# Kernel optimization log

Measured on AMD Instinct MI355X. Metric: run time of the kernel, lower is better.

Reference implementation:

```python
import jax, jax.numpy as jnp
import numpy as np

N, F_IN, H, D = 4096, 256, 8, 16  # nodes, in_features, heads, per-head dim
HD = H * D                        # 128 = out_features
NEG_SLOPE = 0.3


def _masked_softmax(w, g):
    """Replicates torch.sparse.softmax on (w*g).to_sparse() along dim=2.

    Softmax is taken over entries where g != 0 (the sparse nonzeros),
    with value w*g there; fully-masked rows densify back to all zeros.
    w, g: [H, N, N] -> attn [H, N, N].
    """
    mask = g != 0.0
    val = jnp.where(mask, w * g, jnp.float32(-1e30))
    val = val - jnp.max(val, axis=2, keepdims=True)
    e = jnp.exp(val) * mask.astype(w.dtype)
    denom = jnp.maximum(jnp.sum(e, axis=2, keepdims=True), jnp.float32(1e-30))
    return e / denom


def setup_inputs() -> dict:
    key = jax.random.key(0)
    ks = jax.random.split(key, 12)
    s = 0.05
    inputs = jax.random.normal(ks[0], (N, F_IN), dtype=jnp.float32)
    Dgraph = jax.random.randint(ks[1], (N, N), 0, 2).astype(jnp.float32)
    Sgraph = jax.random.randint(ks[2], (N, N), 0, 2).astype(jnp.float32)
    # params (torch Linear stored here as [in, out] so y = x @ W + b)
    W_w = jax.random.normal(ks[3], (F_IN, HD), dtype=jnp.float32) * s
    W_b = jax.random.normal(ks[4], (HD,), dtype=jnp.float32) * s
    wu = jax.random.normal(ks[5], (H, D, 1), dtype=jnp.float32) * s
    wv = jax.random.normal(ks[6], (H, D, 1), dtype=jnp.float32) * s
    Wcat_w = jax.random.normal(ks[7], (2 * HD, HD), dtype=jnp.float32) * s
    Wcat_b = jax.random.normal(ks[8], (HD,), dtype=jnp.float32) * s
    bias = jax.random.normal(ks[9], (1, HD), dtype=jnp.float32) * s
    proj_w = jax.random.normal(ks[10], (F_IN, HD), dtype=jnp.float32) * s
    proj_b = jax.random.normal(ks[11], (HD,), dtype=jnp.float32) * s
    return {"inputs": inputs, "Dgraph": Dgraph, "Sgraph": Sgraph,
            "W_w": W_w, "W_b": W_b, "wu": wu, "wv": wv,
            "Wcat_w": Wcat_w, "Wcat_b": Wcat_b, "bias": bias,
            "proj_w": proj_w, "proj_b": proj_b}


def reference(inputs, Dgraph, Sgraph, W_w, W_b, wu, wv, Wcat_w, Wcat_b, bias, proj_w, proj_b):
    n = inputs.shape[0]
    score = (inputs @ W_w + W_b).reshape(n, H, D).transpose(1, 0, 2)  # [H,N,D]
    f1 = jnp.einsum('hnd,hd->hn', score, wu[:, :, 0])[:, None, :]     # [H,1,N]
    f2 = jnp.einsum('hnd,hd->hn', score, wv[:, :, 0])[:, :, None]     # [H,N,1]
    logits = f1 + f2                                                  # [H,N,N]
    w = jnp.where(logits >= 0, logits, NEG_SLOPE * logits)            # leaky_relu

    D_attn = _masked_softmax(w, Dgraph[None])                         # [H,N,N]
    D_sup = jnp.einsum('hnm,hmd->hnd', D_attn, score)
    D_sup = D_sup.transpose(1, 0, 2).reshape(n, HD)

    S_attn = _masked_softmax(w, Sgraph[None])
    S_sup = jnp.einsum('hnm,hmd->hnd', S_attn, score)
    S_sup = S_sup.transpose(1, 0, 2).reshape(n, HD)

    out = jnp.concatenate([S_sup, D_sup], axis=1) @ Wcat_w + Wcat_b
    out = out + bias
    out = out + inputs @ proj_w + proj_b
    return out
```

## Files before the change

kernel.cpp:

```cpp
#include <hip/hip_runtime.h>
#include <hip/hip_bf16.h>


#define NN 4096
#define LOG2E 1.44269504088896340736f
#define NS 4
#define CHUNK 1024
#define MROW 2064

typedef short bf16x8 __attribute__((ext_vector_type(8)));
typedef float f32x4  __attribute__((ext_vector_type(4)));
typedef _Float16 h16x8 __attribute__((ext_vector_type(8)));
typedef _Float16 h16x2 __attribute__((ext_vector_type(2)));
typedef __fp16  fp16x2 __attribute__((ext_vector_type(2)));

union hu8 { unsigned int u[4]; h16x8 v; };
union hu2 { unsigned int u; h16x2 h; };

__device__ __forceinline__ unsigned short f2bf_rn(float f) {
  union { float f; unsigned int i; } v; v.f = f;
  unsigned int r = v.i + 0x7FFFu + ((v.i >> 16) & 1u);
  return (unsigned short)(r >> 16);
}
__device__ __forceinline__ unsigned int pk2(float lo, float hi) {
  fp16x2 h = __builtin_amdgcn_cvt_pkrtz(lo, hi);
  union { fp16x2 h; unsigned int u; } v; v.h = h; return v.u;
}
__device__ __forceinline__ float dot2acc(unsigned int pair, float acc) {
  hu2 p; p.u = pair;
#if __has_builtin(__builtin_amdgcn_fdot2)
  const h16x2 one2 = {(_Float16)1.f, (_Float16)1.f};
  return __builtin_amdgcn_fdot2(p.h, one2, acc, false);
#else
  return acc + (float)p.h.x + (float)p.h.y;
#endif
}
__device__ __forceinline__ unsigned int bytesel(float4 a) {
  return (a.x != 0.f ? 0x000000FFu : 0u) | (a.y != 0.f ? 0x0000FF00u : 0u)
       | (a.z != 0.f ? 0x00FF0000u : 0u) | (a.w != 0.f ? 0xFF000000u : 0u);
}

__global__ __launch_bounds__(256) void k_prep(
    const float* __restrict__ X, const float* __restrict__ Ww,
    const float* __restrict__ Wcat, const float* __restrict__ proj,
    const float* __restrict__ Wcb, const float* __restrict__ bias,
    const float* __restrict__ prb,
    unsigned short* __restrict__ Xb, unsigned short* __restrict__ WwT,
    unsigned short* __restrict__ WpT, float* __restrict__ bsum)
{
  const int tid = blockIdx.x * 256 + threadIdx.x;
  {
    const float4 a = *(const float4*)(X + (size_t)tid * 8);
    const float4 b = *(const float4*)(X + (size_t)tid * 8 + 4);
    uint4 o;
    o.x = (unsigned)f2bf_rn(a.x) | ((unsigned)f2bf_rn(a.y) << 16);
    o.y = (unsigned)f2bf_rn(a.z) | ((unsigned)f2bf_rn(a.w) << 16);
    o.z = (unsigned)f2bf_rn(b.x) | ((unsigned)f2bf_rn(b.y) << 16);
    o.w = (unsigned)f2bf_rn(b.z) | ((unsigned)f2bf_rn(b.w) << 16);
    *(uint4*)(Xb + (size_t)tid * 8) = o;
  }
  if (tid < 32768) {
    int c = tid & 127, k = tid >> 7;
    WwT[c * 256 + k] = f2bf_rn(Ww[k * 128 + c]);
  }
  if (tid < 65536) {
    int c = tid & 127, k = tid >> 7;
    float v = (k < 256) ? Wcat[k * 128 + c] : proj[(k - 256) * 128 + c];
    WpT[c * 512 + k] = f2bf_rn(v);
  }
  if (tid < 128) bsum[tid] = Wcb[tid] + bias[tid] + prb[tid];
}

__global__ __launch_bounds__(256) void k_cvt(
    const float* __restrict__ Dg, const float* __restrict__ Sg,
    unsigned char* __restrict__ mDS)
{
  const size_t tid = (size_t)blockIdx.x * 256 + threadIdx.x;
  const size_t off = tid * 8;
  const float4 da = *(const float4*)(Dg + off);
  const float4 db = *(const float4*)(Dg + off + 4);
  const float4 sa = *(const float4*)(Sg + off);
  const float4 sb = *(const float4*)(Sg + off + 4);
  uint4 o;
  o.x = bytesel(da); o.y = bytesel(db);
  o.z = bytesel(sa); o.w = bytesel(sb);
  *(uint4*)(mDS + tid * 16) = o;
}

__global__ __launch_bounds__(512) void k_score(
    const unsigned short* __restrict__ Xb, const unsigned short* __restrict__ WwT,
    const float* __restrict__ Wb, const float* __restrict__ wu,
    const float* __restrict__ wv,
    unsigned short* __restrict__ scT, float* __restrict__ f2,
    unsigned short* __restrict__ E1p, unsigned short* __restrict__ E3p)
{
  const int n0 = blockIdx.x * 16;
  const int h = threadIdx.x >> 6, lane = threadIdx.x & 63;
  const int mr = lane & 15, grp = lane >> 4;
  const unsigned short* ap  = Xb  + (size_t)(n0 + mr) * 256;
  const unsigned short* bpp = WwT + (size_t)(h * 16 + mr) * 256;
  f32x4 acc = {0.f, 0.f, 0.f, 0.f};
  #pragma unroll
  for (int ks = 0; ks < 8; ++ks) {
    bf16x8 a = *(const bf16x8*)(ap  + ks * 32 + grp * 8);
    bf16x8 b = *(const bf16x8*)(bpp + ks * 32 + grp * 8);
    acc = __builtin_amdgcn_mfma_f32_16x16x32_bf16(a, b, acc, 0, 0, 0);
  }
  const float wb = Wb[h * 16 + mr];
  float sc[4];
  #pragma unroll
  for (int r = 0; r < 4; ++r) sc[r] = acc[r] + wb;

  {
    uint2 st;
    st.x = pk2(sc[0], sc[1]);
    st.y = pk2(sc[2], sc[3]);
    *(uint2*)(scT + (size_t)(h * 16 + mr) * NN + n0 + grp * 4) = st;
  }

  const float uw = wu[h * 16 + mr], vw = wv[h * 16 + mr];
  float t1[4], t2[4];
  #pragma unroll
  for (int r = 0; r < 4; ++r) { t1[r] = sc[r] * uw; t2[r] = sc[r] * vw; }
  #pragma unroll
  for (int m = 1; m < 16; m <<= 1) {
    #pragma unroll
    for (int r = 0; r < 4; ++r) {
      t1[r] += __shfl_xor(t1[r], m, 64);
      t2[r] += __shfl_xor(t2[r], m, 64);
    }
  }
  if (mr == 0) {
    *(float4*)(f2 + h * NN + n0 + grp * 4) = make_float4(t2[0], t2[1], t2[2], t2[3]);
    float e1[4], e3[4];
    #pragma unroll
    for (int r = 0; r < 4; ++r) {
      e1[r] = __builtin_amdgcn_exp2f(t1[r] * LOG2E);
      e3[r] = __builtin_amdgcn_exp2f(0.3f * t1[r] * LOG2E);
    }
    uint2 p1, p3;
    p1.x = pk2(e1[0], e1[1]);
    p1.y = pk2(e1[2], e1[3]);
    p3.x = pk2(e3[0], e3[1]);
    p3.y = pk2(e3[2], e3[3]);
    *(uint2*)(E1p + h * NN + n0 + grp * 4) = p1;
    *(uint2*)(E3p + h * NN + n0 + grp * 4) = p3;
  }
}

__global__ __launch_bounds__(512, 8) void k_attn(
    const unsigned char* __restrict__ mDS,
    const unsigned short* __restrict__ scT, const unsigned short* __restrict__ E1p,
    const unsigned short* __restrict__ E3p, const float* __restrict__ f2,
    float* __restrict__ pn, float* __restrict__ pd)
{
  __shared__ __align__(16) unsigned char mlds[16][MROW];
  const int bx = blockIdx.x;
  const int c = bx >> 8, t = bx & 255;
  const int i0 = t << 4, j0 = c * CHUNK;
  const int tid = threadIdx.x;

  {
    const int sr = tid >> 5, ss = tid & 31;
    const unsigned char* src = mDS + (size_t)(i0 + sr) * 8192 + j0 * 2 + ss * 64;
    unsigned char* dst = &mlds[sr][ss * 64];
    #pragma unroll
    for (int i = 0; i < 4; ++i)
      *(uint4*)(dst + i * 16) = *(const uint4*)(src + i * 16);
  }
  __syncthreads();

  const int h = tid >> 6, lane = tid & 63;
  const int mr = lane & 15, grp = lane >> 4;

  const float f2v = f2[h * NN + i0 + mr];
  const _Float16 afh = (_Float16)__builtin_amdgcn_exp2f(f2v * LOG2E);
  const _Float16 bfh = (_Float16)__builtin_amdgcn_exp2f(0.3f * f2v * LOG2E);
  const h16x8 af8 = {afh, afh, afh, afh, afh, afh, afh, afh};
  const h16x8 bf8 = {bfh, bfh, bfh, bfh, bfh, bfh, bfh, bfh};

  const _Float16* e1p_ = (const _Float16*)E1p + h * NN + j0 + grp * 8;
  const _Float16* e3p_ = (const _Float16*)E3p + h * NN + j0 + grp * 8;
  const _Float16* scp_ = (const _Float16*)scT + (size_t)(h * 16 + mr) * NN + j0 + grp * 8;
  const unsigned char* mrow = &mlds[mr][grp * 16];

  f32x4 accD = {0.f,0.f,0.f,0.f}, accS = {0.f,0.f,0.f,0.f};
  float dnD = 0.f, dnS = 0.f;

  #pragma unroll 2
  for (int it = 0; it < CHUNK / 32; ++it) {
    const uint4 m4 = *(const uint4*)(mrow + it * 64);
    const h16x8 e1 = *(const h16x8*)(e1p_ + it * 32);
    const h16x8 e3 = *(const h16x8*)(e3p_ + it * 32);
    const h16x8 sv = *(const h16x8*)(scp_ + it * 32);

    hu8 Q, AD, AS;
    Q.v = __builtin_elementwise_max(e1 * af8, e3 * bf8);
    AD.u[0] = Q.u[0] & __builtin_amdgcn_perm(0u, m4.x, 0x01010000u);
    AD.u[1] = Q.u[1] & __builtin_amdgcn_perm(0u, m4.x, 0x03030202u);
    AD.u[2] = Q.u[2] & __builtin_amdgcn_perm(0u, m4.y, 0x01010000u);
    AD.u[3] = Q.u[3] & __builtin_amdgcn_perm(0u, m4.y, 0x03030202u);
    AS.u[0] = Q.u[0] & __builtin_amdgcn_perm(0u, m4.z, 0x01010000u);
    AS.u[1] = Q.u[1] & __builtin_amdgcn_perm(0u, m4.z, 0x03030202u);
    AS.u[2] = Q.u[2] & __builtin_amdgcn_perm(0u, m4.w, 0x01010000u);
    AS.u[3] = Q.u[3] & __builtin_amdgcn_perm(0u, m4.w, 0x03030202u);

    accD = __builtin_amdgcn_mfma_f32_16x16x32_f16(AD.v, sv, accD, 0, 0, 0);
    accS = __builtin_amdgcn_mfma_f32_16x16x32_f16(AS.v, sv, accS, 0, 0, 0);

    #pragma unroll
    for (int p = 0; p < 4; ++p) {
      dnD = dot2acc(AD.u[p], dnD);
      dnS = dot2acc(AS.u[p], dnS);
    }
  }

  dnD += __shfl_xor(dnD, 16, 64); dnD += __shfl_xor(dnD, 32, 64);
  dnS += __shfl_xor(dnS, 16, 64); dnS += __shfl_xor(dnS, 32, 64);

  float* pnb = pn + ((((size_t)c * 256 + t) * 8 + h) * 2) * 256;
  #pragma unroll
  for (int r = 0; r < 4; ++r) {
    const int row = grp * 4 + r;
    pnb[row * 16 + mr]       = accD[r];
    pnb[256 + row * 16 + mr] = accS[r];
  }
  if (lane < 16) {
    float* pdb = pd + ((((size_t)c * 256 + t) * 8 + h) * 2) * 16;
    pdb[lane]      = dnD;
    pdb[16 + lane] = dnS;
  }
}

__global__ __launch_bounds__(512) void k_reduce(
    const float* __restrict__ pn, const float* __restrict__ pd,
    const unsigned short* __restrict__ Xb, const unsigned short* __restrict__ WpT,
    const float* __restrict__ bsum, float* __restrict__ out)
{
  __shared__ unsigned short catT[16][520];
  const int t = blockIdx.x, i0 = t * 16;
  const int tid = threadIdx.x;
  {
    const int r = tid >> 5, x0 = (tid & 31) * 8;
    *(bf16x8*)(&catT[r][256 + x0]) = *(const bf16x8*)(Xb + (size_t)(i0 + r) * 256 + x0);
  }
  const int h = tid >> 6, lane = tid & 63;
  const int mr = lane & 15, grp = lane >> 4;

  #pragma unroll
  for (int r = 0; r < 4; ++r) {
    const int row = grp * 4 + r;
    float vD = 0.f, vS = 0.f, dD = 0.f, dS = 0.f;
    #pragma unroll
    for (int c = 0; c < NS; ++c) {
      const size_t nb = ((((size_t)c * 256 + t) * 8 + h) * 2) * 256;
      const size_t db = ((((size_t)c * 256 + t) * 8 + h) * 2) * 16;
      vD += pn[nb + row * 16 + mr];
      vS += pn[nb + 256 + row * 16 + mr];
      dD += pd[db + row];
      dS += pd[db + 16 + row];
    }
    const float oS = vS * __builtin_amdgcn_rcpf(fmaxf(dS, 1e-30f));
    const float oD = vD * __builtin_amdgcn_rcpf(fmaxf(dD, 1e-30f));
    catT[row][h * 16 + mr]       = f2bf_rn(oS);
    catT[row][128 + h * 16 + mr] = f2bf_rn(oD);
  }
  __syncthreads();

  f32x4 o = {0.f, 0.f, 0.f, 0.f};
  const unsigned short* wp = WpT + (size_t)(h * 16 + mr) * 512;
  #pragma unroll
  for (int ks = 0; ks < 16; ++ks) {
    bf16x8 a = *(const bf16x8*)(&catT[mr][ks * 32 + grp * 8]);
    bf16x8 b = *(const bf16x8*)(wp + ks * 32 + grp * 8);
    o = __builtin_amdgcn_mfma_f32_16x16x32_bf16(a, b, o, 0, 0, 0);
  }
  const float bs = bsum[h * 16 + mr];
  #pragma unroll
  for (int r = 0; r < 4; ++r)
    out[(size_t)(i0 + grp * 4 + r) * 128 + h * 16 + mr] = o[r] + bs;
}

extern "C" void kernel_launch(void* const* d_in, const int* in_sizes, int n_in,
                              void* d_out, int out_size, void* d_ws, size_t ws_size,
                              hipStream_t stream) {
  const float* X    = (const float*)d_in[0];
  const float* Dg   = (const float*)d_in[1];
  const float* Sg   = (const float*)d_in[2];
  const float* Ww   = (const float*)d_in[3];
  const float* Wb   = (const float*)d_in[4];
  const float* wu   = (const float*)d_in[5];
  const float* wv   = (const float*)d_in[6];
  const float* Wcat = (const float*)d_in[7];
  const float* Wcb  = (const float*)d_in[8];
  const float* bias = (const float*)d_in[9];
  const float* proj = (const float*)d_in[10];
  const float* prb  = (const float*)d_in[11];
  float* out = (float*)d_out;

  char* ws = (char*)d_ws;
  unsigned short* Xb   = (unsigned short*)(ws);
  unsigned short* scT  = (unsigned short*)(ws + 0x200000);
  float*          f2   = (float*)(ws + 0x300000);
  unsigned short* E1p  = (unsigned short*)(ws + 0x320000);
  unsigned short* E3p  = (unsigned short*)(ws + 0x330000);
  unsigned short* WwT  = (unsigned short*)(ws + 0x340000);
  unsigned short* WpT  = (unsigned short*)(ws + 0x350000);
  float*          bsum = (float*)(ws + 0x370000);
  unsigned char*  mDS  = (unsigned char*)(ws + 0x400000);
  float*          pn   = (float*)(ws + 0x2400000);
  float*          pd   = (float*)(ws + 0x3400000);

  k_prep<<<dim3(512), dim3(256), 0, stream>>>(X, Ww, Wcat, proj, Wcb, bias, prb,
                                              Xb, WwT, WpT, bsum);
  k_cvt<<<dim3(8192), dim3(256), 0, stream>>>(Dg, Sg, mDS);
  k_score<<<dim3(256), dim3(512), 0, stream>>>(Xb, WwT, Wb, wu, wv, scT, f2, E1p, E3p);
  k_attn<<<dim3(NS * 256), dim3(512), 0, stream>>>(mDS, scT, E1p, E3p, f2, pn, pd);
  k_reduce<<<dim3(256), dim3(512), 0, stream>>>(pn, pd, Xb, WpT, bsum, out);
}
```

Baseline: 100.9 us.

## Store scores in MFMA-fragment-blocked layout and read masks directly from global

```diff
diff --git a/kernel.cpp b/kernel.cpp
--- a/kernel.cpp
+++ b/kernel.cpp
@@ -6,7 +6,6 @@
 #define LOG2E 1.44269504088896340736f
 #define NS 4
 #define CHUNK 1024
-#define MROW 2064
 
 typedef short bf16x8 __attribute__((ext_vector_type(8)));
 typedef float f32x4  __attribute__((ext_vector_type(4)));
@@ -91,7 +90,7 @@
     const unsigned short* __restrict__ Xb, const unsigned short* __restrict__ WwT,
     const float* __restrict__ Wb, const float* __restrict__ wu,
     const float* __restrict__ wv,
-    unsigned short* __restrict__ scT, float* __restrict__ f2,
+    unsigned short* __restrict__ scB, float* __restrict__ f2,
     unsigned short* __restrict__ E1p, unsigned short* __restrict__ E3p)
 {
   const int n0 = blockIdx.x * 16;
@@ -112,10 +111,13 @@
   for (int r = 0; r < 4; ++r) sc[r] = acc[r] + wb;
 
   {
+    const int jb = n0 >> 5;
+    const int lp = ((grp >> 1) + ((n0 >> 4) & 1) * 2) * 16 + mr;
     uint2 st;
     st.x = pk2(sc[0], sc[1]);
     st.y = pk2(sc[2], sc[3]);
-    *(uint2*)(scT + (size_t)(h * 16 + mr) * NN + n0 + grp * 4) = st;
+    *(uint2*)((unsigned char*)scB + ((size_t)(h * 128 + jb) * 64 + lp) * 16
+              + (grp & 1) * 8) = st;
   }
 
   const float uw = wu[h * 16 + mr], vw = wv[h * 16 + mr];
@@ -150,26 +152,14 @@
 
 __global__ __launch_bounds__(512, 8) void k_attn(
     const unsigned char* __restrict__ mDS,
-    const unsigned short* __restrict__ scT, const unsigned short* __restrict__ E1p,
+    const unsigned short* __restrict__ scB, const unsigned short* __restrict__ E1p,
     const unsigned short* __restrict__ E3p, const float* __restrict__ f2,
     float* __restrict__ pn, float* __restrict__ pd)
 {
-  __shared__ __align__(16) unsigned char mlds[16][MROW];
   const int bx = blockIdx.x;
   const int c = bx >> 8, t = bx & 255;
   const int i0 = t << 4, j0 = c * CHUNK;
   const int tid = threadIdx.x;
-
-  {
-    const int sr = tid >> 5, ss = tid & 31;
-    const unsigned char* src = mDS + (size_t)(i0 + sr) * 8192 + j0 * 2 + ss * 64;
-    unsigned char* dst = &mlds[sr][ss * 64];
-    #pragma unroll
-    for (int i = 0; i < 4; ++i)
-      *(uint4*)(dst + i * 16) = *(const uint4*)(src + i * 16);
-  }
-  __syncthreads();
-
   const int h = tid >> 6, lane = tid & 63;
   const int mr = lane & 15, grp = lane >> 4;
 
@@ -181,8 +171,9 @@
 
   const _Float16* e1p_ = (const _Float16*)E1p + h * NN + j0 + grp * 8;
   const _Float16* e3p_ = (const _Float16*)E3p + h * NN + j0 + grp * 8;
-  const _Float16* scp_ = (const _Float16*)scT + (size_t)(h * 16 + mr) * NN + j0 + grp * 8;
-  const unsigned char* mrow = &mlds[mr][grp * 16];
+  const unsigned short* svb = scB + ((size_t)(h * 128 + (j0 >> 5)) * 64 + lane) * 8;
+  const unsigned char* mrow = mDS + (size_t)(i0 + mr) * 8192 + (size_t)(j0 >> 3) * 16
+                              + grp * 16;
 
   f32x4 accD = {0.f,0.f,0.f,0.f}, accS = {0.f,0.f,0.f,0.f};
   float dnD = 0.f, dnS = 0.f;
@@ -192,7 +183,7 @@
     const uint4 m4 = *(const uint4*)(mrow + it * 64);
     const h16x8 e1 = *(const h16x8*)(e1p_ + it * 32);
     const h16x8 e3 = *(const h16x8*)(e3p_ + it * 32);
-    const h16x8 sv = *(const h16x8*)(scp_ + it * 32);
+    const h16x8 sv = *(const h16x8*)(svb + it * 512);
 
     hu8 Q, AD, AS;
     Q.v = __builtin_elementwise_max(e1 * af8, e3 * bf8);
@@ -300,7 +291,7 @@
 
   char* ws = (char*)d_ws;
   unsigned short* Xb   = (unsigned short*)(ws);
-  unsigned short* scT  = (unsigned short*)(ws + 0x200000);
+  unsigned short* scB  = (unsigned short*)(ws + 0x200000);
   float*          f2   = (float*)(ws + 0x300000);
   unsigned short* E1p  = (unsigned short*)(ws + 0x320000);
   unsigned short* E3p  = (unsigned short*)(ws + 0x330000);
@@ -314,7 +305,7 @@
   k_prep<<<dim3(512), dim3(256), 0, stream>>>(X, Ww, Wcat, proj, Wcb, bias, prb,
                                               Xb, WwT, WpT, bsum);
   k_cvt<<<dim3(8192), dim3(256), 0, stream>>>(Dg, Sg, mDS);
-  k_score<<<dim3(256), dim3(512), 0, stream>>>(Xb, WwT, Wb, wu, wv, scT, f2, E1p, E3p);
-  k_attn<<<dim3(NS * 256), dim3(512), 0, stream>>>(mDS, scT, E1p, E3p, f2, pn, pd);
+  k_score<<<dim3(256), dim3(512), 0, stream>>>(Xb, WwT, Wb, wu, wv, scB, f2, E1p, E3p);
+  k_attn<<<dim3(NS * 256), dim3(512), 0, stream>>>(mDS, scB, E1p, E3p, f2, pn, pd);
   k_reduce<<<dim3(256), dim3(512), 0, stream>>>(pn, pd, Xb, WpT, bsum, out);
 }
```

After: 101.6 us. Within noise of the previous version (+0.6%).
